# Performance work log

Hardware: AMD Instinct MI355X
Metric: run time of the kernel (lower is better)

## Reference

```python
import jax, jax.numpy as jnp
import numpy as np

D_MODEL = 1024
NUM_HEADS = 16
D_K = D_MODEL // NUM_HEADS


def setup_inputs() -> dict:
    key = jax.random.key(0)
    ks = jax.random.split(key, 11)
    B, S = 2, 2048
    scale = 1.0 / np.sqrt(D_MODEL)
    inp = {
        'q': jax.random.normal(ks[0], (B, S, D_MODEL), dtype=jnp.float32),
        'k': jax.random.normal(ks[1], (B, S, D_MODEL), dtype=jnp.float32),
        'v': jax.random.normal(ks[2], (B, S, D_MODEL), dtype=jnp.float32),
        'W_q': jax.random.normal(ks[3], (D_MODEL, D_MODEL), dtype=jnp.float32) * scale,
        'b_q': jnp.zeros((D_MODEL,), dtype=jnp.float32),
        'W_k': jax.random.normal(ks[4], (D_MODEL, D_MODEL), dtype=jnp.float32) * scale,
        'b_k': jnp.zeros((D_MODEL,), dtype=jnp.float32),
        'W_v': jax.random.normal(ks[5], (D_MODEL, D_MODEL), dtype=jnp.float32) * scale,
        'b_v': jnp.zeros((D_MODEL,), dtype=jnp.float32),
        'W_o': jax.random.normal(ks[6], (D_MODEL, D_MODEL), dtype=jnp.float32) * scale,
        'b_o': jnp.zeros((D_MODEL,), dtype=jnp.float32),
    }
    return inp


def _split_heads(x):
    # [B, S, D] -> [B, H, S, d_k]
    B, S, _ = x.shape
    return x.reshape(B, S, NUM_HEADS, D_K).transpose(0, 2, 1, 3)


def reference(q, k, v, W_q, b_q, W_k, b_k, W_v, b_v, W_o, b_o):
    # Linear projections (torch Linear: x @ W.T + b)
    qh = _split_heads(q @ W_q.T + b_q)  # [B,H,S,dk]
    kh = _split_heads(k @ W_k.T + b_k)
    vh = _split_heads(v @ W_v.T + b_v)
    scores = jnp.einsum('bhsd,bhtd->bhst', qh, kh) / jnp.sqrt(
        jnp.asarray(D_K, dtype=qh.dtype))  # [B,H,S,S]
    probs = jax.nn.softmax(scores, axis=-1)
    attn = jnp.einsum('bhst,bhtd->bhsd', probs, vh)  # [B,H,S,dk]
    B, H, S, dk = attn.shape
    combined = attn.transpose(0, 2, 1, 3).reshape(B, S, H * dk)  # [B,S,D]
    return combined @ W_o.T + b_o
```

## Files before the change

### kernel.cpp

```cpp
#include <hip/hip_runtime.h>
#include <hip/hip_bf16.h>

typedef __bf16 bf16;
typedef __attribute__((ext_vector_type(4))) __bf16 bf16x4;
typedef __attribute__((ext_vector_type(8))) __bf16 bf16x8;
typedef __attribute__((ext_vector_type(4))) float f32x4;

#define AS1C(p) ((const __attribute__((address_space(1))) void*)(p))
#define AS3(p)  ((__attribute__((address_space(3))) void*)(p))

static constexpr int B_ = 2, S_ = 2048, DM = 1024, H_ = 16, DK = 64;
static constexpr int M_ = B_ * S_;
static constexpr int NW = DM * DM;
static constexpr int NX = M_ * DM;
static constexpr float QSCL = 0.125f * 1.44269504088896340736f;

__device__ __forceinline__ float fast_exp2(float x) {
#if __has_builtin(__builtin_amdgcn_exp2f)
  return __builtin_amdgcn_exp2f(x);
#else
  return exp2f(x);
#endif
}

__global__ __launch_bounds__(256) void cast_all(
    const float* Wq, const float* Wk, const float* Wv, const float* Wo,
    const float* q, const float* k, const float* v,
    bf16* wq, bf16* wk, bf16* wv, bf16* wo,
    bf16* qo, bf16* ko, bf16* vo)
{
  const int z = blockIdx.y;
  const float* in; bf16* out; int n; float s = 1.f;
  switch (z) {
    case 0: in = Wq; out = wq; n = NW; s = QSCL; break;
    case 1: in = Wk; out = wk; n = NW; break;
    case 2: in = Wv; out = wv; n = NW; break;
    case 3: in = Wo; out = wo; n = NW; break;
    case 4: in = q;  out = qo; n = NX; break;
    case 5: in = k;  out = ko; n = NX; break;
    default: in = v; out = vo; n = NX; break;
  }
  const int i = (blockIdx.x * 256 + threadIdx.x) * 8;
  if (i >= n) return;
  f32x4 a = *(const f32x4*)(in + i);
  f32x4 b = *(const f32x4*)(in + i + 4);
  bf16x8 o;
#pragma unroll
  for (int j = 0; j < 4; ++j) { o[j] = (bf16)(a[j] * s); o[4 + j] = (bf16)(b[j] * s); }
  *(bf16x8*)(out + i) = o;
}

__global__ __launch_bounds__(256) void cast_f32_bf16(
    const float* __restrict__ in, bf16* __restrict__ out, int n)
{
  const int i = (blockIdx.x * 256 + threadIdx.x) * 8;
  if (i >= n) return;
  f32x4 a = *(const f32x4*)(in + i);
  f32x4 b = *(const f32x4*)(in + i + 4);
  bf16x8 o;
#pragma unroll
  for (int j = 0; j < 4; ++j) { o[j] = (bf16)a[j]; o[4 + j] = (bf16)b[j]; }
  *(bf16x8*)(out + i) = o;
}

template<int WTM, bool A_BF16, bool OUT_F32>
__device__ __forceinline__ void gemm_body(
    const void* __restrict__ Ain, const bf16* __restrict__ W,
    const float* __restrict__ bias, float bscale, void* __restrict__ Cout,
    bool transv, int M, int N, int K, int bx, int by)
{
  constexpr int BMt = 2 * WTM;
  constexpr int WI  = WTM / 16;
  __shared__ bf16 As[2 * BMt * 32];
  __shared__ bf16 Bs[2 * 128 * 32];

  const int tid  = threadIdx.x;
  const int wave = tid >> 6, lane = tid & 63;
  const int quad = lane >> 4, l16 = lane & 15;
  const int wm = wave >> 1, wn = wave & 1;
  const int row0 = by * BMt;
  const int col0 = bx * 128;

  const int srow  = lane >> 2;
  const int skcol = (lane & 3) * 8;

  f32x4 acc[WI][4] = {};

  for (int k0 = 0; k0 < K; k0 += 64) {
#pragma unroll
    for (int hf = 0; hf < 2; ++hf) {
      const int kb = k0 + hf * 32;
      if constexpr (A_BF16) {
        const bf16* A = (const bf16*)Ain;
#pragma unroll
        for (int c = wave; c < BMt / 16; c += 4)
          __builtin_amdgcn_global_load_lds(
              AS1C(A + (size_t)(row0 + c * 16 + srow) * K + kb + skcol),
              AS3(As + hf * BMt * 32 + c * 16 * 32), 16, 0, 0);
      } else {
        const float* A = (const float*)Ain;
#pragma unroll
        for (int p = 0; p < BMt / 32; ++p) {
          const int idx = p * 256 + tid;
          const int row = idx >> 3, kc = idx & 7;
          f32x4 v = *(const f32x4*)(A + (size_t)(row0 + row) * K + kb + kc * 4);
          bf16x4 o;
#pragma unroll
          for (int j = 0; j < 4; ++j) o[j] = (bf16)v[j];
          *(bf16x4*)(As + hf * BMt * 32 + row * 32 + kc * 4) = o;
        }
      }
#pragma unroll
      for (int i = 0; i < 2; ++i) {
        const int c = wave * 2 + i;
        __builtin_amdgcn_global_load_lds(
            AS1C(W + (size_t)(col0 + c * 16 + srow) * K + kb + skcol),
            AS3(Bs + hf * 128 * 32 + c * 16 * 32), 16, 0, 0);
      }
    }
    __syncthreads();

#pragma unroll
    for (int hf = 0; hf < 2; ++hf) {
      bf16x8 a[WI], bfr[4];
#pragma unroll
      for (int i = 0; i < WI; ++i)
        a[i] = *(const bf16x8*)(As + hf * BMt * 32 + (wm * WTM + i * 16 + l16) * 32 + quad * 8);
#pragma unroll
      for (int j = 0; j < 4; ++j)
        bfr[j] = *(const bf16x8*)(Bs + hf * 128 * 32 + (wn * 64 + j * 16 + l16) * 32 + quad * 8);
#pragma unroll
      for (int i = 0; i < WI; ++i)
#pragma unroll
        for (int j = 0; j < 4; ++j)
          acc[i][j] = __builtin_amdgcn_mfma_f32_16x16x32_bf16(a[i], bfr[j], acc[i][j], 0, 0, 0);
    }
    __syncthreads();
  }

#pragma unroll
  for (int j = 0; j < 4; ++j) {
    const int col = col0 + wn * 64 + j * 16 + l16;
    const float bv = bias[col] * bscale;
    if (!OUT_F32 && transv) {
      const int hh = col >> 6, dd = col & 63;
#pragma unroll
      for (int i = 0; i < WI; ++i) {
        const int row = row0 + wm * WTM + i * 16 + quad * 4;
        const int bb2 = row >> 11, tok = row & 2047;
        bf16x4 o;
#pragma unroll
        for (int r = 0; r < 4; ++r) o[r] = (bf16)(acc[i][j][r] + bv);
        *(bf16x4*)((bf16*)Cout + (((size_t)bb2 * H_ + hh) * DK + dd) * S_ + tok) = o;
      }
    } else {
#pragma unroll
      for (int i = 0; i < WI; ++i) {
#pragma unroll
        for (int r = 0; r < 4; ++r) {
          const int row = row0 + wm * WTM + i * 16 + quad * 4 + r;
          const float val = acc[i][j][r] + bv;
          if constexpr (OUT_F32)
            ((float*)Cout)[(size_t)row * N + col] = val;
          else
            ((bf16*)Cout)[(size_t)row * N + col] = (bf16)val;
        }
      }
    }
  }
}

template<int WTM, bool A_BF16, bool OUT_F32>
__global__ __launch_bounds__(256) void gemm_bt(
    const void* __restrict__ Ain, const bf16* __restrict__ W,
    const float* __restrict__ bias, void* __restrict__ Cout,
    int M, int N, int K)
{
  gemm_body<WTM, A_BF16, OUT_F32>(Ain, W, bias, 1.0f, Cout, false, M, N, K,
                                  blockIdx.x, blockIdx.y);
}

template<bool A_BF16>
__global__ __launch_bounds__(256) void gemm_qkv(
    const void* A0, const void* A1, const void* A2,
    const bf16* __restrict__ Wc,
    const float* b0, const float* b1, const float* b2,
    bf16* C0, bf16* C1, bf16* C2, int M, int N, int K)
{
  const int z = blockIdx.z;
  const void* A = z == 0 ? A0 : (z == 1 ? A1 : A2);
  const float* bias = z == 0 ? b0 : (z == 1 ? b1 : b2);
  const float bscale = z == 0 ? QSCL : 1.0f;
  bf16* C = z == 0 ? C0 : (z == 1 ? C1 : C2);
  gemm_body<64, A_BF16, false>(A, Wc + (size_t)z * NW, bias, bscale, C,
                               z == 2, M, N, K, blockIdx.x, blockIdx.y);
}

__global__ __launch_bounds__(256, 4) void attn_kernel(
    const bf16* __restrict__ Q, const bf16* __restrict__ Kb,
    const bf16* __restrict__ Vtg, bf16* __restrict__ O)
{
  __shared__ bf16 Kt[64 * 72];
  __shared__ bf16 Vt[64 * 72];
  __shared__ bf16 Ps[4 * 16 * 72];

  const int tid  = threadIdx.x;
  const int wave = tid >> 6, lane = tid & 63;
  const int quad = lane >> 4, l16 = lane & 15;
  const int b = blockIdx.z, h = blockIdx.y;
  const int q0 = blockIdx.x * 64 + wave * 16;
  const size_t base  = (size_t)b * S_ * DM + (size_t)h * DK;
  const size_t baseV = ((size_t)b * H_ + h) * DK * S_;

  bf16x8 qf[2];
#pragma unroll
  for (int kt = 0; kt < 2; ++kt)
    qf[kt] = *(const bf16x8*)(Q + base + (size_t)(q0 + l16) * DM + kt * 32 + quad * 8);

  const bool kside = (wave < 2);
  const int srow  = kside ? (tid >> 1) : ((tid - 128) >> 1);
  const int shalf = tid & 1;
  const bf16* gp = kside
      ? (Kb + base + (size_t)srow * DM + shalf * 32)
      : (Vtg + baseV + (size_t)srow * S_ + shalf * 32);
  const size_t gstep = kside ? (size_t)64 * DM : 64;
  bf16* ldst = (kside ? Kt : Vt) + srow * 72 + shalf * 32;

  bf16x8 st[4];
#pragma unroll
  for (int c = 0; c < 4; ++c) st[c] = *(const bf16x8*)(gp + c * 8);
  gp += gstep;

  f32x4 lacc = {0.f, 0.f, 0.f, 0.f};
  f32x4 accO[4] = {};
  bf16* Pw = Ps + wave * 16 * 72;

  for (int it = 0; it < S_ / 64; ++it) {
    __syncthreads();
#pragma unroll
    for (int c = 0; c < 4; ++c) *(bf16x8*)(ldst + c * 8) = st[c];
    __syncthreads();

    if (it + 1 < S_ / 64) {
#pragma unroll
      for (int c = 0; c < 4; ++c) st[c] = *(const bf16x8*)(gp + c * 8);
      gp += gstep;
    }

    f32x4 sc[4];
#pragma unroll
    for (int ct = 0; ct < 4; ++ct) {
      const bf16* kp = Kt + (ct * 16 + l16) * 72 + quad * 8;
      f32x4 a = {0.f, 0.f, 0.f, 0.f};
      a = __builtin_amdgcn_mfma_f32_16x16x32_bf16(*(const bf16x8*)kp,        qf[0], a, 0, 0, 0);
      a = __builtin_amdgcn_mfma_f32_16x16x32_bf16(*(const bf16x8*)(kp + 32), qf[1], a, 0, 0, 0);
      sc[ct] = a;
    }

#pragma unroll
    for (int ct = 0; ct < 4; ++ct) {
      bf16x4 pk;
#pragma unroll
      for (int r = 0; r < 4; ++r) {
        const float p = fast_exp2(sc[ct][r]);
        lacc[r] += p;
        pk[r] = (bf16)p;
      }
      *(bf16x4*)(Pw + l16 * 72 + ct * 16 + quad * 4) = pk;
    }
    bf16x8 pf0 = *(const bf16x8*)(Pw + l16 * 72 + quad * 8);
    bf16x8 pf1 = *(const bf16x8*)(Pw + l16 * 72 + 32 + quad * 8);

#pragma unroll
    for (int dt = 0; dt < 4; ++dt) {
      const bf16* vp = Vt + (dt * 16 + l16) * 72;
      accO[dt] = __builtin_amdgcn_mfma_f32_16x16x32_bf16(
          *(const bf16x8*)(vp + quad * 8),      pf0, accO[dt], 0, 0, 0);
      accO[dt] = __builtin_amdgcn_mfma_f32_16x16x32_bf16(
          *(const bf16x8*)(vp + 32 + quad * 8), pf1, accO[dt], 0, 0, 0);
    }
  }

  float l_s = (lacc[0] + lacc[1]) + (lacc[2] + lacc[3]);
  l_s += __shfl_xor(l_s, 16, 64);
  l_s += __shfl_xor(l_s, 32, 64);
  const float inv = 1.0f / l_s;
#pragma unroll
  for (int dt = 0; dt < 4; ++dt) {
    bf16x4 o;
#pragma unroll
    for (int r = 0; r < 4; ++r) o[r] = (bf16)(accO[dt][r] * inv);
    *(bf16x4*)(O + base + (size_t)(q0 + l16) * DM + dt * 16 + quad * 4) = o;
  }
}

extern "C" void kernel_launch(void* const* d_in, const int* in_sizes, int n_in,
                              void* d_out, int out_size, void* d_ws, size_t ws_size,
                              hipStream_t stream) {
  (void)in_sizes; (void)n_in; (void)out_size;
  const float* q  = (const float*)d_in[0];
  const float* k  = (const float*)d_in[1];
  const float* v  = (const float*)d_in[2];
  const float* Wq = (const float*)d_in[3];
  const float* bq = (const float*)d_in[4];
  const float* Wk = (const float*)d_in[5];
  const float* bk = (const float*)d_in[6];
  const float* Wv = (const float*)d_in[7];
  const float* bvv= (const float*)d_in[8];
  const float* Wo = (const float*)d_in[9];
  const float* bo = (const float*)d_in[10];
  float* out = (float*)d_out;

  char* ws = (char*)d_ws;
  const size_t MB = 1024 * 1024;
  bf16* Qb  = (bf16*)(ws);
  bf16* Kbf = (bf16*)(ws + 8 * MB);
  bf16* Vtg = (bf16*)(ws + 16 * MB);
  bf16* Ab  = (bf16*)(ws + 24 * MB);
  bf16* Wc  = Ab;

  const bool big = ws_size >= 58 * MB;
  bf16* qc  = (bf16*)(ws + 32 * MB);
  bf16* kc  = (bf16*)(ws + 40 * MB);
  bf16* vc  = (bf16*)(ws + 48 * MB);
  bf16* WoC = big ? (bf16*)(ws + 56 * MB) : Qb;

  dim3 bb(256, 1, 1);
  dim3 gqkv(DM / 128, M_ / 128, 3);
  dim3 gout(DM / 128, M_ / 64, 1);

  if (big) {
    cast_all<<<dim3(NX / 2048, 7, 1), bb, 0, stream>>>(
        Wq, Wk, Wv, Wo, q, k, v,
        Wc, Wc + NW, Wc + 2 * NW, WoC, qc, kc, vc);
    gemm_qkv<true><<<gqkv, bb, 0, stream>>>(qc, kc, vc, Wc, bq, bk, bvv,
                                            Qb, Kbf, Vtg, M_, DM, DM);
  } else {
    cast_all<<<dim3(NW / 2048, 3, 1), bb, 0, stream>>>(
        Wq, Wk, Wv, Wo, q, k, v,
        Wc, Wc + NW, Wc + 2 * NW, WoC, nullptr, nullptr, nullptr);
    gemm_qkv<false><<<gqkv, bb, 0, stream>>>(q, k, v, Wc, bq, bk, bvv,
                                             Qb, Kbf, Vtg, M_, DM, DM);
  }

  attn_kernel<<<dim3(S_ / 64, H_, B_), bb, 0, stream>>>(Qb, Kbf, Vtg, Ab);

  if (!big)
    cast_f32_bf16<<<dim3(NW / 2048, 1, 1), bb, 0, stream>>>(Wo, WoC, NW);
  gemm_bt<32, true, true><<<gout, bb, 0, stream>>>(Ab, WoC, bo, out, M_, DM, DM);
}
```

Measured before the change: 234.0 us.

## Prefetch fp32 A tiles in registers and double-buffer attention K/V

The QKV GEMM now always reads fp32 activations directly. It prefetches the next K-tile into registers while the current tile is computed, and the trailing barrier moves to the loop head. The separate full-activation cast kernel and the workspace-size branch are gone. The attention kernel double-buffers K/V tiles in shared memory, which drops one barrier per iteration, and lowers occupancy from 4 to 3 blocks per SM to fit the extra LDS and registers. In exchange it adds register pressure, and the QKV GEMM does more fp32 loads.

```diff
diff --git a/kernel.cpp b/kernel.cpp
--- a/kernel.cpp
+++ b/kernel.cpp
@@ -12,7 +12,6 @@
 static constexpr int B_ = 2, S_ = 2048, DM = 1024, H_ = 16, DK = 64;
 static constexpr int M_ = B_ * S_;
 static constexpr int NW = DM * DM;
-static constexpr int NX = M_ * DM;
 static constexpr float QSCL = 0.125f * 1.44269504088896340736f;
 
 __device__ __forceinline__ float fast_exp2(float x) {
@@ -23,25 +22,14 @@
 #endif
 }
 
-__global__ __launch_bounds__(256) void cast_all(
-    const float* Wq, const float* Wk, const float* Wv, const float* Wo,
-    const float* q, const float* k, const float* v,
-    bf16* wq, bf16* wk, bf16* wv, bf16* wo,
-    bf16* qo, bf16* ko, bf16* vo)
+__global__ __launch_bounds__(256) void cast_w3(
+    const float* Wq, const float* Wk, const float* Wv, bf16* outw)
 {
   const int z = blockIdx.y;
-  const float* in; bf16* out; int n; float s = 1.f;
-  switch (z) {
-    case 0: in = Wq; out = wq; n = NW; s = QSCL; break;
-    case 1: in = Wk; out = wk; n = NW; break;
-    case 2: in = Wv; out = wv; n = NW; break;
-    case 3: in = Wo; out = wo; n = NW; break;
-    case 4: in = q;  out = qo; n = NX; break;
-    case 5: in = k;  out = ko; n = NX; break;
-    default: in = v; out = vo; n = NX; break;
-  }
+  const float* in = z == 0 ? Wq : (z == 1 ? Wk : Wv);
+  const float s = z == 0 ? QSCL : 1.0f;
+  bf16* out = outw + (size_t)z * NW;
   const int i = (blockIdx.x * 256 + threadIdx.x) * 8;
-  if (i >= n) return;
   f32x4 a = *(const f32x4*)(in + i);
   f32x4 b = *(const f32x4*)(in + i + 4);
   bf16x8 o;
@@ -51,10 +39,9 @@
 }
 
 __global__ __launch_bounds__(256) void cast_f32_bf16(
-    const float* __restrict__ in, bf16* __restrict__ out, int n)
+    const float* __restrict__ in, bf16* __restrict__ out)
 {
   const int i = (blockIdx.x * 256 + threadIdx.x) * 8;
-  if (i >= n) return;
   f32x4 a = *(const f32x4*)(in + i);
   f32x4 b = *(const f32x4*)(in + i + 4);
   bf16x8 o;
@@ -84,41 +71,68 @@
   const int srow  = lane >> 2;
   const int skcol = (lane & 3) * 8;
 
+  const int arow  = tid >> 1;
+  const int ak16  = (tid & 1) * 16;
+  const float* agp = nullptr;
+  f32x4 pre[8];
+  if constexpr (!A_BF16) {
+    agp = (const float*)Ain + (size_t)(row0 + arow) * K + ak16;
+#pragma unroll
+    for (int hf = 0; hf < 2; ++hf)
+#pragma unroll
+      for (int c = 0; c < 4; ++c)
+        pre[hf * 4 + c] = *(const f32x4*)(agp + hf * 32 + c * 4);
+  }
+
   f32x4 acc[WI][4] = {};
 
   for (int k0 = 0; k0 < K; k0 += 64) {
-#pragma unroll
-    for (int hf = 0; hf < 2; ++hf) {
-      const int kb = k0 + hf * 32;
-      if constexpr (A_BF16) {
-        const bf16* A = (const bf16*)Ain;
+    __syncthreads();
+    if constexpr (A_BF16) {
+      const bf16* A = (const bf16*)Ain;
+#pragma unroll
+      for (int hf = 0; hf < 2; ++hf)
 #pragma unroll
         for (int c = wave; c < BMt / 16; c += 4)
           __builtin_amdgcn_global_load_lds(
-              AS1C(A + (size_t)(row0 + c * 16 + srow) * K + kb + skcol),
+              AS1C(A + (size_t)(row0 + c * 16 + srow) * K + k0 + hf * 32 + skcol),
               AS3(As + hf * BMt * 32 + c * 16 * 32), 16, 0, 0);
-      } else {
-        const float* A = (const float*)Ain;
-#pragma unroll
-        for (int p = 0; p < BMt / 32; ++p) {
-          const int idx = p * 256 + tid;
-          const int row = idx >> 3, kc = idx & 7;
-          f32x4 v = *(const f32x4*)(A + (size_t)(row0 + row) * K + kb + kc * 4);
-          bf16x4 o;
-#pragma unroll
-          for (int j = 0; j < 4; ++j) o[j] = (bf16)v[j];
-          *(bf16x4*)(As + hf * BMt * 32 + row * 32 + kc * 4) = o;
+    } else {
+#pragma unroll
+      for (int hf = 0; hf < 2; ++hf) {
+        bf16x8 w0, w1;
+#pragma unroll
+        for (int j = 0; j < 4; ++j) {
+          w0[j]     = (bf16)pre[hf * 4 + 0][j];
+          w0[4 + j] = (bf16)pre[hf * 4 + 1][j];
+          w1[j]     = (bf16)pre[hf * 4 + 2][j];
+          w1[4 + j] = (bf16)pre[hf * 4 + 3][j];
         }
-      }
+        bf16* dst = As + hf * BMt * 32 + arow * 32 + ak16;
+        *(bf16x8*)dst = w0;
+        *(bf16x8*)(dst + 8) = w1;
+      }
+    }
+#pragma unroll
+    for (int hf = 0; hf < 2; ++hf)
 #pragma unroll
       for (int i = 0; i < 2; ++i) {
         const int c = wave * 2 + i;
         __builtin_amdgcn_global_load_lds(
-            AS1C(W + (size_t)(col0 + c * 16 + srow) * K + kb + skcol),
+            AS1C(W + (size_t)(col0 + c * 16 + srow) * K + k0 + hf * 32 + skcol),
             AS3(Bs + hf * 128 * 32 + c * 16 * 32), 16, 0, 0);
       }
-    }
     __syncthreads();
+
+    if constexpr (!A_BF16) {
+      if (k0 + 64 < K) {
+#pragma unroll
+        for (int hf = 0; hf < 2; ++hf)
+#pragma unroll
+          for (int c = 0; c < 4; ++c)
+            pre[hf * 4 + c] = *(const f32x4*)(agp + k0 + 64 + hf * 32 + c * 4);
+      }
+    }
 
 #pragma unroll
     for (int hf = 0; hf < 2; ++hf) {
@@ -135,7 +149,6 @@
         for (int j = 0; j < 4; ++j)
           acc[i][j] = __builtin_amdgcn_mfma_f32_16x16x32_bf16(a[i], bfr[j], acc[i][j], 0, 0, 0);
     }
-    __syncthreads();
   }
 
 #pragma unroll
@@ -180,28 +193,27 @@
                                   blockIdx.x, blockIdx.y);
 }
 
-template<bool A_BF16>
 __global__ __launch_bounds__(256) void gemm_qkv(
-    const void* A0, const void* A1, const void* A2,
+    const float* A0, const float* A1, const float* A2,
     const bf16* __restrict__ Wc,
     const float* b0, const float* b1, const float* b2,
     bf16* C0, bf16* C1, bf16* C2, int M, int N, int K)
 {
   const int z = blockIdx.z;
-  const void* A = z == 0 ? A0 : (z == 1 ? A1 : A2);
+  const float* A = z == 0 ? A0 : (z == 1 ? A1 : A2);
   const float* bias = z == 0 ? b0 : (z == 1 ? b1 : b2);
   const float bscale = z == 0 ? QSCL : 1.0f;
   bf16* C = z == 0 ? C0 : (z == 1 ? C1 : C2);
-  gemm_body<64, A_BF16, false>(A, Wc + (size_t)z * NW, bias, bscale, C,
-                               z == 2, M, N, K, blockIdx.x, blockIdx.y);
-}
-
-__global__ __launch_bounds__(256, 4) void attn_kernel(
+  gemm_body<64, false, false>(A, Wc + (size_t)z * NW, bias, bscale, C,
+                              z == 2, M, N, K, blockIdx.x, blockIdx.y);
+}
+
+__global__ __launch_bounds__(256, 3) void attn_kernel(
     const bf16* __restrict__ Q, const bf16* __restrict__ Kb,
     const bf16* __restrict__ Vtg, bf16* __restrict__ O)
 {
-  __shared__ bf16 Kt[64 * 72];
-  __shared__ bf16 Vt[64 * 72];
+  __shared__ bf16 Kt[2][64 * 72];
+  __shared__ bf16 Vt[2][64 * 72];
   __shared__ bf16 Ps[4 * 16 * 72];
 
   const int tid  = threadIdx.x;
@@ -224,9 +236,15 @@
       ? (Kb + base + (size_t)srow * DM + shalf * 32)
       : (Vtg + baseV + (size_t)srow * S_ + shalf * 32);
   const size_t gstep = kside ? (size_t)64 * DM : 64;
-  bf16* ldst = (kside ? Kt : Vt) + srow * 72 + shalf * 32;
+  bf16* ldst0 = (kside ? Kt[0] : Vt[0]) + srow * 72 + shalf * 32;
+  bf16* ldst1 = (kside ? Kt[1] : Vt[1]) + srow * 72 + shalf * 32;
 
   bf16x8 st[4];
+#pragma unroll
+  for (int c = 0; c < 4; ++c) st[c] = *(const bf16x8*)(gp + c * 8);
+#pragma unroll
+  for (int c = 0; c < 4; ++c) *(bf16x8*)(ldst0 + c * 8) = st[c];
+  gp += gstep;
 #pragma unroll
   for (int c = 0; c < 4; ++c) st[c] = *(const bf16x8*)(gp + c * 8);
   gp += gstep;
@@ -235,22 +253,29 @@
   f32x4 accO[4] = {};
   bf16* Pw = Ps + wave * 16 * 72;
 
-  for (int it = 0; it < S_ / 64; ++it) {
+  constexpr int NIT = S_ / 64;
+  for (int it = 0; it < NIT; ++it) {
+    const int bsel = it & 1;
     __syncthreads();
-#pragma unroll
-    for (int c = 0; c < 4; ++c) *(bf16x8*)(ldst + c * 8) = st[c];
-    __syncthreads();
-
-    if (it + 1 < S_ / 64) {
-#pragma unroll
-      for (int c = 0; c < 4; ++c) st[c] = *(const bf16x8*)(gp + c * 8);
-      gp += gstep;
-    }
+
+    if (it + 1 < NIT) {
+      bf16* dst = bsel ? ldst0 : ldst1;
+#pragma unroll
+      for (int c = 0; c < 4; ++c) *(bf16x8*)(dst + c * 8) = st[c];
+      if (it + 2 < NIT) {
+#pragma unroll
+        for (int c = 0; c < 4; ++c) st[c] = *(const bf16x8*)(gp + c * 8);
+        gp += gstep;
+      }
+    }
+
+    const bf16* Kc = Kt[bsel];
+    const bf16* Vc = Vt[bsel];
 
     f32x4 sc[4];
 #pragma unroll
     for (int ct = 0; ct < 4; ++ct) {
-      const bf16* kp = Kt + (ct * 16 + l16) * 72 + quad * 8;
+      const bf16* kp = Kc + (ct * 16 + l16) * 72 + quad * 8;
       f32x4 a = {0.f, 0.f, 0.f, 0.f};
       a = __builtin_amdgcn_mfma_f32_16x16x32_bf16(*(const bf16x8*)kp,        qf[0], a, 0, 0, 0);
       a = __builtin_amdgcn_mfma_f32_16x16x32_bf16(*(const bf16x8*)(kp + 32), qf[1], a, 0, 0, 0);
@@ -273,7 +298,7 @@
 
 #pragma unroll
     for (int dt = 0; dt < 4; ++dt) {
-      const bf16* vp = Vt + (dt * 16 + l16) * 72;
+      const bf16* vp = Vc + (dt * 16 + l16) * 72;
       accO[dt] = __builtin_amdgcn_mfma_f32_16x16x32_bf16(
           *(const bf16x8*)(vp + quad * 8),      pf0, accO[dt], 0, 0, 0);
       accO[dt] = __builtin_amdgcn_mfma_f32_16x16x32_bf16(
@@ -297,7 +322,7 @@
 extern "C" void kernel_launch(void* const* d_in, const int* in_sizes, int n_in,
                               void* d_out, int out_size, void* d_ws, size_t ws_size,
                               hipStream_t stream) {
-  (void)in_sizes; (void)n_in; (void)out_size;
+  (void)in_sizes; (void)n_in; (void)out_size; (void)ws_size;
   const float* q  = (const float*)d_in[0];
   const float* k  = (const float*)d_in[1];
   const float* v  = (const float*)d_in[2];
@@ -316,36 +341,21 @@
   bf16* Qb  = (bf16*)(ws);
   bf16* Kbf = (bf16*)(ws + 8 * MB);
   bf16* Vtg = (bf16*)(ws + 16 * MB);
+  bf16* Wc  = (bf16*)(ws + 24 * MB);
   bf16* Ab  = (bf16*)(ws + 24 * MB);
-  bf16* Wc  = Ab;
-
-  const bool big = ws_size >= 58 * MB;
-  bf16* qc  = (bf16*)(ws + 32 * MB);
-  bf16* kc  = (bf16*)(ws + 40 * MB);
-  bf16* vc  = (bf16*)(ws + 48 * MB);
-  bf16* WoC = big ? (bf16*)(ws + 56 * MB) : Qb;
+  bf16* WoC = (bf16*)(ws + 8 * MB);
 
   dim3 bb(256, 1, 1);
-  dim3 gqkv(DM / 128, M_ / 128, 3);
-  dim3 gout(DM / 128, M_ / 64, 1);
-
-  if (big) {
-    cast_all<<<dim3(NX / 2048, 7, 1), bb, 0, stream>>>(
-        Wq, Wk, Wv, Wo, q, k, v,
-        Wc, Wc + NW, Wc + 2 * NW, WoC, qc, kc, vc);
-    gemm_qkv<true><<<gqkv, bb, 0, stream>>>(qc, kc, vc, Wc, bq, bk, bvv,
-                                            Qb, Kbf, Vtg, M_, DM, DM);
-  } else {
-    cast_all<<<dim3(NW / 2048, 3, 1), bb, 0, stream>>>(
-        Wq, Wk, Wv, Wo, q, k, v,
-        Wc, Wc + NW, Wc + 2 * NW, WoC, nullptr, nullptr, nullptr);
-    gemm_qkv<false><<<gqkv, bb, 0, stream>>>(q, k, v, Wc, bq, bk, bvv,
-                                             Qb, Kbf, Vtg, M_, DM, DM);
-  }
+
+  cast_w3<<<dim3(NW / 2048, 3, 1), bb, 0, stream>>>(Wq, Wk, Wv, Wc);
+
+  gemm_qkv<<<dim3(DM / 128, M_ / 128, 3), bb, 0, stream>>>(
+      q, k, v, Wc, bq, bk, bvv, Qb, Kbf, Vtg, M_, DM, DM);
 
   attn_kernel<<<dim3(S_ / 64, H_, B_), bb, 0, stream>>>(Qb, Kbf, Vtg, Ab);
 
-  if (!big)
-    cast_f32_bf16<<<dim3(NW / 2048, 1, 1), bb, 0, stream>>>(Wo, WoC, NW);
-  gemm_bt<32, true, true><<<gout, bb, 0, stream>>>(Ab, WoC, bo, out, M_, DM, DM);
-}
+  cast_f32_bf16<<<dim3(NW / 2048, 1, 1), bb, 0, stream>>>(Wo, WoC);
+
+  gemm_bt<32, true, true><<<dim3(DM / 128, M_ / 64, 1), bb, 0, stream>>>(
+      Ab, WoC, bo, out, M_, DM, DM);
+}
```

After: 251.8 us. 1.08x slower.
